# Optimization experiments

Hardware: AMD Instinct MI355X
Metric: run time of the kernel (lower is better)

The kernel has to match this reference:

```python
import jax, jax.numpy as jnp
import numpy as np
from jax import lax


def setup_inputs() -> dict:
    key = jax.random.key(0)
    k1, k2, k3 = jax.random.split(key, 3)
    B, T, D, H = 128, 1024, 512, 512
    x = jax.random.normal(k1, (B, T, D), dtype=jnp.float32)
    # scaled init to keep tanh out of hard saturation
    W_ih = jax.random.normal(k2, (D, H), dtype=jnp.float32) / np.sqrt(D)
    W_hh = jax.random.normal(k3, (H, H), dtype=jnp.float32) / np.sqrt(H)
    b = jnp.zeros((H,), dtype=jnp.float32)
    return {"x": x, "W_ih": W_ih, "W_hh": W_hh, "b": b}


def reference(x, W_ih, W_hh, b):
    # Vanilla RNN: h_t = tanh(x_t @ W_ih + h_{t-1} @ W_hh + b)
    # return_sequences=False -> final hidden state (batch, hidden)
    B = x.shape[0]
    H = W_hh.shape[0]
    # Precompute the large input-to-hidden projection for all timesteps at once.
    xp = jnp.einsum('btd,dh->bth', x, W_ih) + b  # (B, T, H)
    xp_t = jnp.swapaxes(xp, 0, 1)                # (T, B, H) for scan over time

    def step(h, xp_step):
        h_new = jnp.tanh(xp_step + h @ W_hh)
        return h_new, None

    h0 = jnp.zeros((B, H), dtype=x.dtype)
    h_final, _ = lax.scan(step, h0, xp_t)
    return h_final
```

## Files before the change

### kernel.cpp

```cpp
#include <hip/hip_runtime.h>
#include <hip/hip_fp16.h>

typedef _Float16 half8 __attribute__((ext_vector_type(8)));
typedef _Float16 half4v __attribute__((ext_vector_type(4)));
typedef float floatx4 __attribute__((ext_vector_type(4)));

constexpr int BN = 128;
constexpr int T  = 1024;
constexpr int D  = 512;
constexpr int H  = 512;

constexpr size_t OFF_WIHT  = 0;
constexpr size_t OFF_WHHT  = 524288;
constexpr size_t OFF_HX    = 1048576;
constexpr size_t OFF_FLAGS = 1048576 + 262144;
constexpr size_t OFF_XP    = 2097152;

__device__ __forceinline__ float fast_tanh(float x) {
    float e = __expf(2.0f * x);
    return 1.0f - 2.0f / (e + 1.0f);
}

__global__ __launch_bounds__(256) void prep_transpose(
    const float* __restrict__ Wih, const float* __restrict__ Whh,
    _Float16* __restrict__ WihT, _Float16* __restrict__ WhhT,
    int* __restrict__ flags)
{
    if (blockIdx.x == 0 && blockIdx.y == 0 && blockIdx.z == 0 && threadIdx.x < 16)
        flags[threadIdx.x * 16] = 0;

    __shared__ float tile[32][33];
    const float* src = (blockIdx.z == 0) ? Wih : Whh;
    _Float16* dst    = (blockIdx.z == 0) ? WihT : WhhT;
    const int tx = threadIdx.x & 31;
    const int ty = threadIdx.x >> 5;
    const int kbase = blockIdx.y * 32;
    const int nbase = blockIdx.x * 32;
    for (int r = 0; r < 4; ++r)
        tile[ty + r * 8][tx] = src[(size_t)(kbase + ty + r * 8) * 512 + nbase + tx];
    __syncthreads();
    for (int r = 0; r < 4; ++r)
        dst[(size_t)(nbase + ty + r * 8) * 512 + kbase + tx] =
            (_Float16)tile[tx][ty + r * 8];
}

__global__ __launch_bounds__(256) void xp_gemm(
    const float* __restrict__ x, const _Float16* __restrict__ WT,
    const float* __restrict__ bias, _Float16* __restrict__ xp)
{
    __shared__ _Float16 As[128][40];
    __shared__ _Float16 Bs[128][40];
    const int tid  = threadIdx.x;
    const int lane = tid & 63;
    const int w    = tid >> 6;
    const int wm   = w & 1, wn = w >> 1;
    const int l15  = lane & 15, q = lane >> 4;
    const size_t mbase = (size_t)blockIdx.y * 128;
    const int    nbase = blockIdx.x * 128;

    floatx4 acc[4][4];
    for (int i = 0; i < 4; ++i)
        for (int j = 0; j < 4; ++j)
            acc[i][j] = (floatx4){0.f, 0.f, 0.f, 0.f};

    for (int kt = 0; kt < 16; ++kt) {
        const int k0 = kt * 32;
        {
            const int k4 = (tid & 7) * 4;
            const int row0 = tid >> 3;
            for (int r = 0; r < 4; ++r) {
                const int row = row0 + r * 32;
                const float4 v = *(const float4*)&x[(mbase + row) * D + k0 + k4];
                half4v hv;
                hv[0] = (_Float16)v.x; hv[1] = (_Float16)v.y;
                hv[2] = (_Float16)v.z; hv[3] = (_Float16)v.w;
                *(half4v*)&As[row][k4] = hv;
            }
        }
        {
            const int k8 = (tid & 3) * 8;
            const int n0 = tid >> 2;
            for (int r = 0; r < 2; ++r) {
                const int n = n0 + r * 64;
                *(half8*)&Bs[n][k8] =
                    *(const half8*)&WT[(size_t)(nbase + n) * D + k0 + k8];
            }
        }
        __syncthreads();
        half8 a[4], b[4];
        for (int i = 0; i < 4; ++i)
            a[i] = *(const half8*)&As[wm * 64 + i * 16 + l15][q * 8];
        for (int j = 0; j < 4; ++j)
            b[j] = *(const half8*)&Bs[wn * 64 + j * 16 + l15][q * 8];
        for (int i = 0; i < 4; ++i)
            for (int j = 0; j < 4; ++j)
                acc[i][j] = __builtin_amdgcn_mfma_f32_16x16x32_f16(
                    a[i], b[j], acc[i][j], 0, 0, 0);
        __syncthreads();
    }
    float bc[4];
    for (int j = 0; j < 4; ++j)
        bc[j] = bias[nbase + wn * 64 + j * 16 + l15];
    for (int i = 0; i < 4; ++i)
        for (int r = 0; r < 4; ++r) {
            const size_t row = mbase + wm * 64 + i * 16 + q * 4 + r;
            const int b_row = (int)(row >> 10);
            const int tt    = (int)(row & 1023);
            _Float16* dst = &xp[((size_t)tt * BN + b_row) * H];
            for (int j = 0; j < 4; ++j) {
                const int col = nbase + wn * 64 + j * 16 + l15;
                dst[col] = (_Float16)(acc[i][j][r] + bc[j]);
            }
        }
}

__global__ __launch_bounds__(512, 2) void rnn_scan(
    const _Float16* __restrict__ xp, const _Float16* __restrict__ WT,
    float* __restrict__ out, _Float16* __restrict__ hx, int* __restrict__ flags)
{
    __shared__ _Float16 hbuf[2][16 * 512];

    const int bid  = blockIdx.x;
    const int half = bid >> 3;
    const int g    = bid & 7;
    const int peer = bid ^ 8;
    const int tid  = threadIdx.x;
    const int lane = tid & 63;
    const int w    = tid >> 6;
    const int l15  = lane & 15;
    const int q    = lane >> 4;

    const int hoff = half * 4096;
    const int poff = hoff ^ 4096;

    const int nbase = half * 256 + w * 32;
    const _Float16* wr0 = WT + (size_t)(nbase + 0  + l15) * H + q * 8;
    const _Float16* wr1 = WT + (size_t)(nbase + 16 + l15) * H + q * 8;

    half8 wa[16][2];
#pragma unroll
    for (int j = 0; j < 16; ++j) {
        const int c = (j < 8) ? (half * 8 + j) : ((half ^ 1) * 8 + (j - 8));
        wa[j][0] = *(const half8*)&wr0[c * 32];
        wa[j][1] = *(const half8*)&wr1[c * 32];
        asm volatile("" : "+a"(wa[j][0]), "+a"(wa[j][1]));
    }

    {
        const _Float16* x0 = xp + ((size_t)g * 16 + l15) * H;
#pragma unroll
        for (int i = 0; i < 4; ++i) {
            const int hid = w * 64 + i * 16 + q * 4;
            half4v v = *(const half4v*)&x0[hid];
            half4v hn;
#pragma unroll
            for (int r = 0; r < 4; ++r)
                hn[r] = (_Float16)fast_tanh((float)v[r]);
            const int c = hid >> 5, qr = (hid >> 3) & 3, lo = hid & 7;
            *(half4v*)&hbuf[1][((c * 4 + qr) * 16 + l15) * 8 + lo] = hn;
        }
        __syncthreads();
    }

    const _Float16* xlane = xp + ((size_t)g * 16 + l15) * H + nbase + q * 4;
    const int ebase = (w * 4 + (q >> 1)) * 128 + l15 * 8 + (q & 1) * 4;

    for (int t = 1; t < T; ++t) {
        const _Float16* hb = hbuf[t & 1];

        const _Float16* xt = xlane + (size_t)t * (BN * H);
        const half4v xpv0 = *(const half4v*)&xt[0];
        const half4v xpv1 = *(const half4v*)&xt[16];

        int f = 0x7fffffff;
        if (t >= 2 && lane == 0)
            f = __hip_atomic_load(&flags[peer * 16], __ATOMIC_RELAXED,
                                  __HIP_MEMORY_SCOPE_AGENT);

        const _Float16* hbo = hb + hoff + (q * 16 + l15) * 8;
        half8 hfA[8];
#pragma unroll
        for (int c8 = 0; c8 < 8; ++c8)
            hfA[c8] = *(const half8*)&hbo[c8 * 512];
        floatx4 accA0 = (floatx4){0.f,0.f,0.f,0.f};
        floatx4 accA1 = (floatx4){0.f,0.f,0.f,0.f};
#pragma unroll
        for (int c8 = 0; c8 < 8; ++c8) {
            accA0 = __builtin_amdgcn_mfma_f32_16x16x32_f16(wa[c8][0], hfA[c8], accA0, 0, 0, 0);
            accA1 = __builtin_amdgcn_mfma_f32_16x16x32_f16(wa[c8][1], hfA[c8], accA1, 0, 0, 0);
        }

        if (t >= 2) {
            if (lane == 0) {
                while (f < t - 1) {
                    __builtin_amdgcn_s_sleep(1);
                    f = __hip_atomic_load(&flags[peer * 16], __ATOMIC_ACQUIRE,
                                          __HIP_MEMORY_SCOPE_AGENT);
                }
            }
            const size_t sb = ((size_t)((t & 1) * 8 + g) * 2 + (half ^ 1)) * 4096;
            unsigned long long* src = (unsigned long long*)(hx + sb);
            unsigned long long d0 = __hip_atomic_load(&src[tid * 2 + 0],
                                    __ATOMIC_RELAXED, __HIP_MEMORY_SCOPE_AGENT);
            unsigned long long d1 = __hip_atomic_load(&src[tid * 2 + 1],
                                    __ATOMIC_RELAXED, __HIP_MEMORY_SCOPE_AGENT);
            unsigned long long* dl = (unsigned long long*)&hbuf[t & 1][poff];
            dl[tid * 2 + 0] = d0;
            dl[tid * 2 + 1] = d1;
            __syncthreads();
        }

        const _Float16* hbp = hb + poff + (q * 16 + l15) * 8;
        half8 hfB[8];
#pragma unroll
        for (int c8 = 0; c8 < 8; ++c8)
            hfB[c8] = *(const half8*)&hbp[c8 * 512];
        floatx4 accB0 = (floatx4){0.f,0.f,0.f,0.f};
        floatx4 accB1 = (floatx4){0.f,0.f,0.f,0.f};
#pragma unroll
        for (int c8 = 0; c8 < 8; ++c8) {
            accB0 = __builtin_amdgcn_mfma_f32_16x16x32_f16(wa[8 + c8][0], hfB[c8], accB0, 0, 0, 0);
            accB1 = __builtin_amdgcn_mfma_f32_16x16x32_f16(wa[8 + c8][1], hfB[c8], accB1, 0, 0, 0);
        }

        const floatx4 acc0 = accA0 + accB0;
        const floatx4 acc1 = accA1 + accB1;

        if (t < T - 1) {
            _Float16* ho  = hbuf[(t + 1) & 1];
            _Float16* hxo = hx + ((size_t)(((t + 1) & 1) * 8 + g) * 2 + half) * 4096;
            half4v hn0, hn1;
#pragma unroll
            for (int r = 0; r < 4; ++r) {
                hn0[r] = (_Float16)fast_tanh(acc0[r] + (float)xpv0[r]);
                hn1[r] = (_Float16)fast_tanh(acc1[r] + (float)xpv1[r]);
            }
            *(half4v*)&ho[hoff + ebase]       = hn0;
            *(half4v*)&ho[hoff + ebase + 256] = hn1;
            __hip_atomic_store((unsigned long long*)hxo + (ebase >> 2),
                               __builtin_bit_cast(unsigned long long, hn0),
                               __ATOMIC_RELAXED, __HIP_MEMORY_SCOPE_AGENT);
            __hip_atomic_store((unsigned long long*)hxo + ((ebase + 256) >> 2),
                               __builtin_bit_cast(unsigned long long, hn1),
                               __ATOMIC_RELAXED, __HIP_MEMORY_SCOPE_AGENT);
            __syncthreads();
            if (tid == 0)
                __hip_atomic_store(&flags[bid * 16], t, __ATOMIC_RELEASE,
                                   __HIP_MEMORY_SCOPE_AGENT);
        } else {
            float4 o0, o1;
            o0.x = fast_tanh(acc0[0] + (float)xpv0[0]);
            o0.y = fast_tanh(acc0[1] + (float)xpv0[1]);
            o0.z = fast_tanh(acc0[2] + (float)xpv0[2]);
            o0.w = fast_tanh(acc0[3] + (float)xpv0[3]);
            o1.x = fast_tanh(acc1[0] + (float)xpv1[0]);
            o1.y = fast_tanh(acc1[1] + (float)xpv1[1]);
            o1.z = fast_tanh(acc1[2] + (float)xpv1[2]);
            o1.w = fast_tanh(acc1[3] + (float)xpv1[3]);
            float* ob = &out[((size_t)g * 16 + l15) * H + nbase + q * 4];
            *(float4*)&ob[0]  = o0;
            *(float4*)&ob[16] = o1;
        }
    }
}

extern "C" void kernel_launch(void* const* d_in, const int* in_sizes, int n_in,
                              void* d_out, int out_size, void* d_ws, size_t ws_size,
                              hipStream_t stream)
{
    const float* x   = (const float*)d_in[0];
    const float* Wih = (const float*)d_in[1];
    const float* Whh = (const float*)d_in[2];
    const float* b   = (const float*)d_in[3];
    float* out = (float*)d_out;

    char* ws = (char*)d_ws;
    _Float16* WihT = (_Float16*)(ws + OFF_WIHT);
    _Float16* WhhT = (_Float16*)(ws + OFF_WHHT);
    _Float16* hx   = (_Float16*)(ws + OFF_HX);
    int*      flags = (int*)(ws + OFF_FLAGS);
    _Float16* xp   = (_Float16*)(ws + OFF_XP);

    prep_transpose<<<dim3(16, 16, 2), 256, 0, stream>>>(Wih, Whh, WihT, WhhT, flags);
    xp_gemm<<<dim3(4, 1024), 256, 0, stream>>>(x, WihT, b, xp);
    rnn_scan<<<16, 512, 0, stream>>>(xp, WhhT, out, hx, flags);
}
```

Before: 3.620 ms.

## Read peer hidden half directly from global into MFMA operands, drop LDS staging barrier

Each block now keeps only its own half of the hidden state in LDS. The peer half is loaded straight from the global exchange buffer into registers for the second MFMA chain, which removes the per-step LDS copy and one __syncthreads. Every lane now polls the peer flag itself, and the flag stores and loads are relaxed instead of release/acquire. Ordering relies on a fake data dependency (f>>31 folded into the address) rather than real memory fences. The t=1 exchange is also seeded by publishing flag 0 after initialisation. All lanes now issue global atomic loads, and the weaker memory ordering risks reading stale data.

```diff
diff --git a/kernel.cpp b/kernel.cpp
--- a/kernel.cpp
+++ b/kernel.cpp
@@ -21,13 +21,15 @@
     return 1.0f - 2.0f / (e + 1.0f);
 }
 
+struct u64x2_s { unsigned long long a, b; };
+
 __global__ __launch_bounds__(256) void prep_transpose(
     const float* __restrict__ Wih, const float* __restrict__ Whh,
     _Float16* __restrict__ WihT, _Float16* __restrict__ WhhT,
     int* __restrict__ flags)
 {
     if (blockIdx.x == 0 && blockIdx.y == 0 && blockIdx.z == 0 && threadIdx.x < 16)
-        flags[threadIdx.x * 16] = 0;
+        flags[threadIdx.x * 16] = -1;
 
     __shared__ float tile[32][33];
     const float* src = (blockIdx.z == 0) ? Wih : Whh;
@@ -118,21 +120,19 @@
     const _Float16* __restrict__ xp, const _Float16* __restrict__ WT,
     float* __restrict__ out, _Float16* __restrict__ hx, int* __restrict__ flags)
 {
-    __shared__ _Float16 hbuf[2][16 * 512];
+    __shared__ _Float16 hbuf[2][4096];
 
     const int bid  = blockIdx.x;
     const int half = bid >> 3;
     const int g    = bid & 7;
-    const int peer = bid ^ 8;
+    const int peer16 = (bid ^ 8) * 16;
+    const int bid16  = bid * 16;
     const int tid  = threadIdx.x;
     const int lane = tid & 63;
     const int w    = tid >> 6;
     const int l15  = lane & 15;
     const int q    = lane >> 4;
 
-    const int hoff = half * 4096;
-    const int poff = hoff ^ 4096;
-
     const int nbase = half * 256 + w * 32;
     const _Float16* wr0 = WT + (size_t)(nbase + 0  + l15) * H + q * 8;
     const _Float16* wr1 = WT + (size_t)(nbase + 16 + l15) * H + q * 8;
@@ -146,106 +146,106 @@
         asm volatile("" : "+a"(wa[j][0]), "+a"(wa[j][1]));
     }
 
+    const int ebase = ((w * 4 + (q >> 1)) * 16 + l15) * 8 + (q & 1) * 4;
+
     {
-        const _Float16* x0 = xp + ((size_t)g * 16 + l15) * H;
-#pragma unroll
-        for (int i = 0; i < 4; ++i) {
-            const int hid = w * 64 + i * 16 + q * 4;
-            half4v v = *(const half4v*)&x0[hid];
-            half4v hn;
-#pragma unroll
-            for (int r = 0; r < 4; ++r)
-                hn[r] = (_Float16)fast_tanh((float)v[r]);
-            const int c = hid >> 5, qr = (hid >> 3) & 3, lo = hid & 7;
-            *(half4v*)&hbuf[1][((c * 4 + qr) * 16 + l15) * 8 + lo] = hn;
-        }
+        const _Float16* x0 = xp + ((size_t)g * 16 + l15) * H + nbase + q * 4;
+        half4v v0 = *(const half4v*)&x0[0];
+        half4v v1 = *(const half4v*)&x0[16];
+        half4v hn0, hn1;
+#pragma unroll
+        for (int r = 0; r < 4; ++r) {
+            hn0[r] = (_Float16)fast_tanh((float)v0[r]);
+            hn1[r] = (_Float16)fast_tanh((float)v1[r]);
+        }
+        _Float16* hxo = hx + ((size_t)(1 * 8 + g) * 2 + half) * 4096;
+        __hip_atomic_store((unsigned long long*)hxo + (ebase >> 2),
+                           __builtin_bit_cast(unsigned long long, hn0),
+                           __ATOMIC_RELAXED, __HIP_MEMORY_SCOPE_AGENT);
+        __hip_atomic_store((unsigned long long*)hxo + ((ebase + 256) >> 2),
+                           __builtin_bit_cast(unsigned long long, hn1),
+                           __ATOMIC_RELAXED, __HIP_MEMORY_SCOPE_AGENT);
+        *(half4v*)&hbuf[1][ebase]       = hn0;
+        *(half4v*)&hbuf[1][ebase + 256] = hn1;
         __syncthreads();
+        if (tid == 0)
+            __hip_atomic_store(&flags[bid16], 0, __ATOMIC_RELAXED,
+                               __HIP_MEMORY_SCOPE_AGENT);
     }
 
     const _Float16* xlane = xp + ((size_t)g * 16 + l15) * H + nbase + q * 4;
-    const int ebase = (w * 4 + (q >> 1)) * 128 + l15 * 8 + (q & 1) * 4;
+    const int poff64 = q * 32 + l15 * 2;
 
     for (int t = 1; t < T; ++t) {
-        const _Float16* hb = hbuf[t & 1];
+        int f = __hip_atomic_load(&flags[peer16], __ATOMIC_RELAXED,
+                                  __HIP_MEMORY_SCOPE_AGENT);
+        __builtin_amdgcn_sched_barrier(0);
 
         const _Float16* xt = xlane + (size_t)t * (BN * H);
         const half4v xpv0 = *(const half4v*)&xt[0];
         const half4v xpv1 = *(const half4v*)&xt[16];
 
-        int f = 0x7fffffff;
-        if (t >= 2 && lane == 0)
-            f = __hip_atomic_load(&flags[peer * 16], __ATOMIC_RELAXED,
-                                  __HIP_MEMORY_SCOPE_AGENT);
-
-        const _Float16* hbo = hb + hoff + (q * 16 + l15) * 8;
+        const _Float16* hbo = &hbuf[t & 1][(q * 16 + l15) * 8];
         half8 hfA[8];
 #pragma unroll
         for (int c8 = 0; c8 < 8; ++c8)
             hfA[c8] = *(const half8*)&hbo[c8 * 512];
-        floatx4 accA0 = (floatx4){0.f,0.f,0.f,0.f};
-        floatx4 accA1 = (floatx4){0.f,0.f,0.f,0.f};
+        floatx4 acc0 = (floatx4){0.f,0.f,0.f,0.f};
+        floatx4 acc1 = (floatx4){0.f,0.f,0.f,0.f};
 #pragma unroll
         for (int c8 = 0; c8 < 8; ++c8) {
-            accA0 = __builtin_amdgcn_mfma_f32_16x16x32_f16(wa[c8][0], hfA[c8], accA0, 0, 0, 0);
-            accA1 = __builtin_amdgcn_mfma_f32_16x16x32_f16(wa[c8][1], hfA[c8], accA1, 0, 0, 0);
-        }
-
-        if (t >= 2) {
-            if (lane == 0) {
-                while (f < t - 1) {
-                    __builtin_amdgcn_s_sleep(1);
-                    f = __hip_atomic_load(&flags[peer * 16], __ATOMIC_ACQUIRE,
-                                          __HIP_MEMORY_SCOPE_AGENT);
-                }
-            }
-            const size_t sb = ((size_t)((t & 1) * 8 + g) * 2 + (half ^ 1)) * 4096;
-            unsigned long long* src = (unsigned long long*)(hx + sb);
-            unsigned long long d0 = __hip_atomic_load(&src[tid * 2 + 0],
+            acc0 = __builtin_amdgcn_mfma_f32_16x16x32_f16(wa[c8][0], hfA[c8], acc0, 0, 0, 0);
+            acc1 = __builtin_amdgcn_mfma_f32_16x16x32_f16(wa[c8][1], hfA[c8], acc1, 0, 0, 0);
+        }
+
+        if (f < t - 1) {
+            do {
+                __builtin_amdgcn_s_sleep(1);
+                f = __hip_atomic_load(&flags[peer16], __ATOMIC_RELAXED,
+                                      __HIP_MEMORY_SCOPE_AGENT);
+            } while (f < t - 1);
+        }
+        asm volatile("" : "+v"(f));
+
+        const unsigned long long* ps64 = (const unsigned long long*)hx
+            + ((size_t)((t & 1) * 8 + g) * 2 + (half ^ 1)) * 1024
+            + poff64 + (f >> 31);
+        half8 hfB[8];
+#pragma unroll
+        for (int c8 = 0; c8 < 8; ++c8) {
+            unsigned long long d0 = __hip_atomic_load(&ps64[c8 * 128 + 0],
                                     __ATOMIC_RELAXED, __HIP_MEMORY_SCOPE_AGENT);
-            unsigned long long d1 = __hip_atomic_load(&src[tid * 2 + 1],
+            unsigned long long d1 = __hip_atomic_load(&ps64[c8 * 128 + 1],
                                     __ATOMIC_RELAXED, __HIP_MEMORY_SCOPE_AGENT);
-            unsigned long long* dl = (unsigned long long*)&hbuf[t & 1][poff];
-            dl[tid * 2 + 0] = d0;
-            dl[tid * 2 + 1] = d1;
-            __syncthreads();
-        }
-
-        const _Float16* hbp = hb + poff + (q * 16 + l15) * 8;
-        half8 hfB[8];
-#pragma unroll
-        for (int c8 = 0; c8 < 8; ++c8)
-            hfB[c8] = *(const half8*)&hbp[c8 * 512];
-        floatx4 accB0 = (floatx4){0.f,0.f,0.f,0.f};
-        floatx4 accB1 = (floatx4){0.f,0.f,0.f,0.f};
+            hfB[c8] = __builtin_bit_cast(half8, u64x2_s{d0, d1});
+        }
+
 #pragma unroll
         for (int c8 = 0; c8 < 8; ++c8) {
-            accB0 = __builtin_amdgcn_mfma_f32_16x16x32_f16(wa[8 + c8][0], hfB[c8], accB0, 0, 0, 0);
-            accB1 = __builtin_amdgcn_mfma_f32_16x16x32_f16(wa[8 + c8][1], hfB[c8], accB1, 0, 0, 0);
-        }
-
-        const floatx4 acc0 = accA0 + accB0;
-        const floatx4 acc1 = accA1 + accB1;
+            acc0 = __builtin_amdgcn_mfma_f32_16x16x32_f16(wa[8 + c8][0], hfB[c8], acc0, 0, 0, 0);
+            acc1 = __builtin_amdgcn_mfma_f32_16x16x32_f16(wa[8 + c8][1], hfB[c8], acc1, 0, 0, 0);
+        }
 
         if (t < T - 1) {
-            _Float16* ho  = hbuf[(t + 1) & 1];
-            _Float16* hxo = hx + ((size_t)(((t + 1) & 1) * 8 + g) * 2 + half) * 4096;
             half4v hn0, hn1;
 #pragma unroll
             for (int r = 0; r < 4; ++r) {
                 hn0[r] = (_Float16)fast_tanh(acc0[r] + (float)xpv0[r]);
                 hn1[r] = (_Float16)fast_tanh(acc1[r] + (float)xpv1[r]);
             }
-            *(half4v*)&ho[hoff + ebase]       = hn0;
-            *(half4v*)&ho[hoff + ebase + 256] = hn1;
+            _Float16* hxo = hx + ((size_t)(((t + 1) & 1) * 8 + g) * 2 + half) * 4096;
             __hip_atomic_store((unsigned long long*)hxo + (ebase >> 2),
                                __builtin_bit_cast(unsigned long long, hn0),
                                __ATOMIC_RELAXED, __HIP_MEMORY_SCOPE_AGENT);
             __hip_atomic_store((unsigned long long*)hxo + ((ebase + 256) >> 2),
                                __builtin_bit_cast(unsigned long long, hn1),
                                __ATOMIC_RELAXED, __HIP_MEMORY_SCOPE_AGENT);
+            _Float16* ho = hbuf[(t + 1) & 1];
+            *(half4v*)&ho[ebase]       = hn0;
+            *(half4v*)&ho[ebase + 256] = hn1;
             __syncthreads();
             if (tid == 0)
-                __hip_atomic_store(&flags[bid * 16], t, __ATOMIC_RELEASE,
+                __hip_atomic_store(&flags[bid16], t, __ATOMIC_RELAXED,
                                    __HIP_MEMORY_SCOPE_AGENT);
         } else {
             float4 o0, o1;
```

Measured after the change: 3.574 ms. About the same (-1.3%).
